# Kernel tuning notes

Measured on AMD Instinct MI355X. Metric: run time of the kernel, lower is better.

Reference implementation:

```python
import jax, jax.numpy as jnp
import numpy as np

N_NODES = 50000


def _sage_conv(x, src, dst, Wl, bl, Wr):
    # mean-aggregate source features onto targets (PyG SAGEConv, aggr='mean')
    msg = x[src]                                             # [E, C_in] gather
    s = jax.ops.segment_sum(msg, dst, num_segments=N_NODES)  # [N, C_in]
    cnt = jax.ops.segment_sum(jnp.ones((src.shape[0],), x.dtype), dst,
                              num_segments=N_NODES)          # [N]
    agg = s / jnp.maximum(cnt, 1.0)[:, None]
    # out = lin_l(agg) + lin_r(x); bias only on lin_l
    return agg @ Wl.T + bl + x @ Wr.T


def setup_inputs() -> dict:
    key = jax.random.key(0)
    ks = jax.random.split(key, 8)
    in_c, hid_c, out_c = 128, 128, 64
    n_edges = 800000
    x = jax.random.normal(ks[0], (N_NODES, in_c), dtype=jnp.float32)
    edge_index = jax.random.randint(ks[1], (2, n_edges), 0, N_NODES, dtype=jnp.int64)
    sc = lambda k, shp: jax.random.normal(k, shp, dtype=jnp.float32) / np.sqrt(shp[1])
    return {
        "x": x,
        "edge_index": edge_index,
        "W1l": sc(ks[2], (hid_c, in_c)),
        "b1l": jnp.zeros((hid_c,), jnp.float32),
        "W1r": sc(ks[3], (hid_c, in_c)),
        "W2l": sc(ks[4], (out_c, hid_c)),
        "b2l": jnp.zeros((out_c,), jnp.float32),
        "W2r": sc(ks[5], (out_c, hid_c)),
    }


def reference(x, edge_index, W1l, b1l, W1r, W2l, b2l, W2r):
    src, dst = edge_index[0], edge_index[1]
    h = jax.nn.relu(_sage_conv(x, src, dst, W1l, b1l, W1r))
    # dropout(p=0.5) is identity at inference (training=False)
    return _sage_conv(h, src, dst, W2l, b2l, W2r)
```

## Files before the change

### kernel.cpp

```cpp
#include <hip/hip_runtime.h>
#include <hip/hip_bf16.h>

#define N_NODES 50000
#define N_EDGES 800000
#define N_BUCKETS 196
#define BUCKET_CAP 8192
#define POISON 0xAAAAAAAAu

#define XCVT_BLK 6250
#define WCVT_BLK 48
#define EPB 2048
#define BKT_BLK 391

typedef __attribute__((ext_vector_type(8))) short short8;
typedef __attribute__((ext_vector_type(4))) float floatx4;

static __device__ __forceinline__ float bf16_lo(unsigned int v) {
  union { unsigned int u; float f; } c; c.u = v << 16; return c.f;
}
static __device__ __forceinline__ float bf16_hi(unsigned int v) {
  union { unsigned int u; float f; } c; c.u = v & 0xffff0000u; return c.f;
}
static __device__ __forceinline__ unsigned short f32_to_bf16_rne(float f) {
  union { float f; unsigned int u; } c; c.f = f;
  unsigned int u = c.u;
  unsigned int r = (u + 0x7fffu + ((u >> 16) & 1u)) >> 16;
  return (unsigned short)r;
}
static __device__ __forceinline__ unsigned int pack2(float a, float b) {
  return (unsigned int)f32_to_bf16_rne(a) | ((unsigned int)f32_to_bf16_rne(b) << 16);
}
static __device__ __forceinline__ uint2 pack4(float4 v) {
  return (uint2){pack2(v.x, v.y), pack2(v.z, v.w)};
}
static __device__ __forceinline__ void accum8(float* acc, uint4 v) {
  acc[0] += bf16_lo(v.x); acc[1] += bf16_hi(v.x);
  acc[2] += bf16_lo(v.y); acc[3] += bf16_hi(v.y);
  acc[4] += bf16_lo(v.z); acc[5] += bf16_hi(v.z);
  acc[6] += bf16_lo(v.w); acc[7] += bf16_hi(v.w);
}

__global__ __launch_bounds__(256) void prep_bucket_kernel(
    const float4* __restrict__ x4, uint2* __restrict__ xb4,
    const float4* __restrict__ w1l4, const float4* __restrict__ w1r4,
    const float4* __restrict__ w2l4, const float4* __restrict__ w2r4,
    uint2* __restrict__ o1l, uint2* __restrict__ o1r,
    uint2* __restrict__ o2l, uint2* __restrict__ o2r,
    const int* __restrict__ src, const int* __restrict__ dst,
    unsigned int* __restrict__ bcur, unsigned int* __restrict__ ebuf) {
  __shared__ int hist[N_BUCKETS];
  __shared__ int base[N_BUCKETS];
  const int b = blockIdx.x, tid = threadIdx.x;
  if (b < XCVT_BLK) {
    int i = b * 256 + tid;
    xb4[i] = pack4(x4[i]);
    return;
  }
  if (b < XCVT_BLK + WCVT_BLK) {
    int j = (b - XCVT_BLK) * 256 + tid;
    const float4* in; uint2* out; int o2, NJ;
    if (j < 4096)       { in = w1l4; out = o1l; o2 = j;         NJ = 128; }
    else if (j < 8192)  { in = w1r4; out = o1r; o2 = j - 4096;  NJ = 128; }
    else if (j < 10240) { in = w2l4; out = o2l; o2 = j - 8192;  NJ = 64; }
    else                { in = w2r4; out = o2r; o2 = j - 10240; NJ = 64; }
    int half = o2 & 1;
    int rest = o2 >> 1;
    int col  = rest % NJ;
    int qk   = rest / NJ;
    int quad = qk & 3, kb = qk >> 2;
    out[o2] = pack4(in[col * 32 + kb * 8 + quad * 2 + half]);
    return;
  }
  const int eb = b - XCVT_BLK - WCVT_BLK;
  for (int i = tid; i < N_BUCKETS; i += 256) hist[i] = 0;
  __syncthreads();
  const int e0 = eb * EPB;
  int bk[8], rk[8];
  unsigned int pk[8];
  bool val[8];
  #pragma unroll
  for (int k = 0; k < 8; ++k) {
    int e = e0 + k * 256 + tid;
    val[k] = (e < N_EDGES);
    if (val[k]) {
      int d = dst[e], s = src[e];
      bk[k] = d >> 8;
      pk[k] = ((unsigned int)(d & 255) << 16) | (unsigned int)s;
      rk[k] = atomicAdd(&hist[bk[k]], 1);
    }
  }
  __syncthreads();
  for (int i = tid; i < N_BUCKETS; i += 256) {
    int h = hist[i];
    base[i] = h ? (int)(atomicAdd(&bcur[i], (unsigned int)h) - POISON) : 0;
  }
  __syncthreads();
  #pragma unroll
  for (int k = 0; k < 8; ++k) {
    if (val[k]) {
      unsigned int p = (unsigned int)(base[bk[k]] + rk[k]);
      if (p < BUCKET_CAP) ebuf[(size_t)bk[k] * BUCKET_CAP + p] = pk[k];
    }
  }
}

__global__ __launch_bounds__(512) void local_csr_kernel(
    const unsigned int* __restrict__ ebuf, const unsigned int* __restrict__ bcur,
    int* __restrict__ start_g, int* __restrict__ cnt_g, int* __restrict__ eidx) {
  const int b = blockIdx.x;
  int nb = (int)(bcur[b] - POISON);
  nb = max(0, min(nb, BUCKET_CAP));
  __shared__ int cnt[256];
  __shared__ int loff[256];
  __shared__ int ws[4];
  if (threadIdx.x < 256) cnt[threadIdx.x] = 0;
  __syncthreads();
  const unsigned int* eb = ebuf + (size_t)b * BUCKET_CAP;
  for (int i = threadIdx.x; i < nb; i += 512)
    atomicAdd(&cnt[eb[i] >> 16], 1);
  __syncthreads();
  const int t256 = threadIdx.x & 255;
  const int lane = threadIdx.x & 63, wid = (threadIdx.x >> 6) & 3;
  int v = cnt[t256];
  int incl = v;
  #pragma unroll
  for (int d = 1; d < 64; d <<= 1) {
    int t = __shfl_up(incl, d, 64);
    if (lane >= d) incl += t;
  }
  if (threadIdx.x < 256 && lane == 63) ws[wid] = incl;
  __syncthreads();
  int add = 0;
  #pragma unroll
  for (int w = 0; w < 4; ++w) if (w < wid) add += ws[w];
  int excl = add + incl - v;
  if (threadIdx.x < 256) {
    loff[t256] = excl;
    int node = b * 256 + t256;
    if (node < N_NODES) {
      start_g[node] = b * BUCKET_CAP + excl;
      cnt_g[node] = v;
    }
  }
  __syncthreads();
  for (int i = threadIdx.x; i < nb; i += 512) {
    unsigned int p = eb[i];
    int pos = atomicAdd(&loff[p >> 16], 1);
    eidx[(size_t)b * BUCKET_CAP + pos] = (int)(p & 0xffffu);
  }
}

__global__ __launch_bounds__(256) void agg_gemm_kernel(
    const uint4* __restrict__ xb4,
    const int* __restrict__ start_g, const int* __restrict__ cnt_g,
    const int* __restrict__ eidx,
    const unsigned short* __restrict__ W1l, const unsigned short* __restrict__ W1r,
    const float* __restrict__ b1,
    const unsigned short* __restrict__ W2l, const unsigned short* __restrict__ W2r,
    const float* __restrict__ b2,
    unsigned short* __restrict__ z, unsigned short* __restrict__ rbuf) {
  __shared__ unsigned short lds_a[64 * 136];
  __shared__ unsigned short lds_x[64 * 136];
  const int tid = threadIdx.x, lane = tid & 63, wave = tid >> 6;
  const int quad = lane >> 4, r16 = lane & 15;
  const int cg = wave & 1, tw = wave >> 1;
  const int col0 = cg * 64;
  const int n0 = blockIdx.x * 64;

  #pragma unroll
  for (int k = 0; k < 4; ++k) {
    int idx = k * 256 + tid;
    int row = idx >> 4, col = idx & 15;
    int gr = n0 + row; if (gr >= N_NODES) gr = N_NODES - 1;
    ((uint4*)lds_x)[row * 17 + col] = xb4[(size_t)gr * 16 + col];
  }

  const int l16 = tid & 15;
  const int grp = tid >> 4;
  #pragma unroll 1
  for (int nn = 0; nn < 4; ++nn) {
    int row = nn * 16 + grp;
    int node = n0 + row;
    float acc[8];
    #pragma unroll
    for (int t = 0; t < 8; ++t) acc[t] = 0.f;
    int c = 0;
    if (node < N_NODES) {
      int e0 = start_g[node];
      c = cnt_g[node];
      int e1 = e0 + c;
      int e = e0;
      for (; e + 8 <= e1; e += 8) {
        int s[8];
        #pragma unroll
        for (int k = 0; k < 8; ++k) s[k] = eidx[e + k];
        uint4 v[8];
        #pragma unroll
        for (int k = 0; k < 8; ++k) v[k] = xb4[(size_t)s[k] * 16 + l16];
        #pragma unroll
        for (int k = 0; k < 8; ++k) accum8(acc, v[k]);
      }
      if (e + 4 <= e1) {
        int s[4];
        #pragma unroll
        for (int k = 0; k < 4; ++k) s[k] = eidx[e + k];
        uint4 v[4];
        #pragma unroll
        for (int k = 0; k < 4; ++k) v[k] = xb4[(size_t)s[k] * 16 + l16];
        #pragma unroll
        for (int k = 0; k < 4; ++k) accum8(acc, v[k]);
        e += 4;
      }
      for (; e < e1; ++e)
        accum8(acc, xb4[(size_t)eidx[e] * 16 + l16]);
    }
    float inv = 1.0f / fmaxf((float)c, 1.0f);
    uint4 o;
    o.x = pack2(acc[0] * inv, acc[1] * inv);
    o.y = pack2(acc[2] * inv, acc[3] * inv);
    o.z = pack2(acc[4] * inv, acc[5] * inv);
    o.w = pack2(acc[6] * inv, acc[7] * inv);
    *(uint4*)(lds_a + row * 136 + l16 * 8) = o;
  }
  __syncthreads();

  const unsigned short* As[2] = {lds_a, lds_x};
  const unsigned short* Ws[2] = {W1l, W1r};
  floatx4 acc1[2][4] = {};
  #pragma unroll
  for (int rt = 0; rt < 2; ++rt) {
    int lrow = tw * 32 + rt * 16;
    #pragma unroll
    for (int s = 0; s < 2; ++s) {
      const unsigned short* Ar = As[s] + (lrow + r16) * 136 + quad * 8;
      #pragma unroll
      for (int kb = 0; kb < 4; ++kb) {
        short8 a = *(const short8*)(Ar + kb * 32);
        const unsigned short* Wf = Ws[s] + ((size_t)(kb * 4 + quad) * 128) * 8;
        #pragma unroll
        for (int c = 0; c < 4; ++c) {
          short8 bfr = *(const short8*)(Wf + (size_t)(col0 + c * 16 + r16) * 8);
          acc1[rt][c] = __builtin_amdgcn_mfma_f32_16x16x32_bf16(a, bfr, acc1[rt][c], 0, 0, 0);
        }
      }
    }
  }
  __syncthreads();

  #pragma unroll
  for (int rt = 0; rt < 2; ++rt) {
    int lrow0 = tw * 32 + rt * 16 + quad * 4;
    #pragma unroll
    for (int c = 0; c < 4; ++c) {
      int j = col0 + c * 16 + r16;
      float bv = b1[j];
      #pragma unroll
      for (int r = 0; r < 4; ++r)
        lds_a[(lrow0 + r) * 136 + j] = f32_to_bf16_rne(fmaxf(acc1[rt][c][r] + bv, 0.f));
    }
  }
  __syncthreads();

  const unsigned short* W = cg ? W2r : W2l;
  unsigned short* outp = cg ? rbuf : z;
  #pragma unroll
  for (int rt = 0; rt < 2; ++rt) {
    int lrow = tw * 32 + rt * 16;
    floatx4 acc[4] = {};
    const unsigned short* la = lds_a + (lrow + r16) * 136 + quad * 8;
    #pragma unroll
    for (int kb = 0; kb < 4; ++kb) {
      short8 a = *(const short8*)(la + kb * 32);
      const unsigned short* Wf = W + ((size_t)(kb * 4 + quad) * 64) * 8;
      #pragma unroll
      for (int c = 0; c < 4; ++c) {
        short8 bfr = *(const short8*)(Wf + (size_t)(c * 16 + r16) * 8);
        acc[c] = __builtin_amdgcn_mfma_f32_16x16x32_bf16(a, bfr, acc[c], 0, 0, 0);
      }
    }
    int orow0 = n0 + lrow + quad * 4;
    #pragma unroll
    for (int c = 0; c < 4; ++c) {
      int j = c * 16 + r16;
      float bv = cg ? b2[j] : 0.f;
      #pragma unroll
      for (int r = 0; r < 4; ++r) {
        int node = orow0 + r;
        if (node < N_NODES)
          outp[(size_t)node * 64 + j] = f32_to_bf16_rne(acc[c][r] + bv);
      }
    }
  }
}

__global__ __launch_bounds__(256) void final_agg_kernel(
    const uint4* __restrict__ z4, const uint4* __restrict__ r4,
    const int* __restrict__ start_g, const int* __restrict__ cnt_g,
    const int* __restrict__ eidx, float* __restrict__ outp) {
  const int l8 = threadIdx.x & 7;
  const int node = blockIdx.x * 32 + (threadIdx.x >> 3);
  if (node >= N_NODES) return;
  int e0 = start_g[node];
  int c = cnt_g[node];
  int e1 = e0 + c;

  float acc[8];
  #pragma unroll
  for (int t = 0; t < 8; ++t) acc[t] = 0.f;

  int e = e0;
  for (; e + 8 <= e1; e += 8) {
    int s[8];
    #pragma unroll
    for (int k = 0; k < 8; ++k) s[k] = eidx[e + k];
    uint4 v[8];
    #pragma unroll
    for (int k = 0; k < 8; ++k) v[k] = z4[(size_t)s[k] * 8 + l8];
    #pragma unroll
    for (int k = 0; k < 8; ++k) accum8(acc, v[k]);
  }
  if (e + 4 <= e1) {
    int s[4];
    #pragma unroll
    for (int k = 0; k < 4; ++k) s[k] = eidx[e + k];
    uint4 v[4];
    #pragma unroll
    for (int k = 0; k < 4; ++k) v[k] = z4[(size_t)s[k] * 8 + l8];
    #pragma unroll
    for (int k = 0; k < 4; ++k) accum8(acc, v[k]);
    e += 4;
  }
  for (; e < e1; ++e)
    accum8(acc, z4[(size_t)eidx[e] * 8 + l8]);

  float inv = 1.0f / fmaxf((float)c, 1.0f);
  uint4 rv = r4[(size_t)node * 8 + l8];
  float4* op = (float4*)(outp + (size_t)node * 64 + l8 * 8);
  float4 a, b;
  a.x = acc[0] * inv + bf16_lo(rv.x); a.y = acc[1] * inv + bf16_hi(rv.x);
  a.z = acc[2] * inv + bf16_lo(rv.y); a.w = acc[3] * inv + bf16_hi(rv.y);
  b.x = acc[4] * inv + bf16_lo(rv.z); b.y = acc[5] * inv + bf16_hi(rv.z);
  b.z = acc[6] * inv + bf16_lo(rv.w); b.w = acc[7] * inv + bf16_hi(rv.w);
  op[0] = a; op[1] = b;
}

extern "C" void kernel_launch(void* const* d_in, const int* in_sizes, int n_in,
                              void* d_out, int out_size, void* d_ws, size_t ws_size,
                              hipStream_t stream) {
  (void)in_sizes; (void)n_in; (void)out_size; (void)ws_size;
  const float* x   = (const float*)d_in[0];
  const int*   ei  = (const int*)d_in[1];
  const float* W1l = (const float*)d_in[2];
  const float* b1l = (const float*)d_in[3];
  const float* W1r = (const float*)d_in[4];
  const float* W2l = (const float*)d_in[5];
  const float* b2l = (const float*)d_in[6];
  const float* W2r = (const float*)d_in[7];
  const int* src = ei;
  const int* dst = ei + N_EDGES;

  char* ws = (char*)d_ws;
  size_t p = 0;
  auto alloc = [&](size_t bytes) {
    char* q = ws + p;
    p = (p + bytes + 255) & ~(size_t)255;
    return q;
  };
  unsigned int* bcur = (unsigned int*)alloc((size_t)N_BUCKETS * 4);
  int* start_g = (int*)alloc((size_t)N_NODES * 4);
  int* cnt_g   = (int*)alloc((size_t)N_NODES * 4);
  unsigned int* ebuf = (unsigned int*)alloc((size_t)N_BUCKETS * BUCKET_CAP * 4);
  int* eidx    = (int*)alloc((size_t)N_BUCKETS * BUCKET_CAP * 4);
  unsigned short* xb   = (unsigned short*)alloc((size_t)N_NODES * 128 * 2);
  unsigned short* zb   = (unsigned short*)alloc((size_t)N_NODES * 64 * 2);
  unsigned short* rb   = (unsigned short*)alloc((size_t)N_NODES * 64 * 2);
  unsigned short* w1lb = (unsigned short*)alloc(128 * 128 * 2);
  unsigned short* w1rb = (unsigned short*)alloc(128 * 128 * 2);
  unsigned short* w2lb = (unsigned short*)alloc(64 * 128 * 2);
  unsigned short* w2rb = (unsigned short*)alloc(64 * 128 * 2);

  prep_bucket_kernel<<<XCVT_BLK + WCVT_BLK + BKT_BLK, 256, 0, stream>>>(
      (const float4*)x, (uint2*)xb,
      (const float4*)W1l, (const float4*)W1r, (const float4*)W2l, (const float4*)W2r,
      (uint2*)w1lb, (uint2*)w1rb, (uint2*)w2lb, (uint2*)w2rb,
      src, dst, bcur, (unsigned int*)ebuf);
  local_csr_kernel<<<N_BUCKETS, 512, 0, stream>>>(
      (const unsigned int*)ebuf, bcur, start_g, cnt_g, eidx);
  agg_gemm_kernel<<<(N_NODES + 63) / 64, 256, 0, stream>>>(
      (const uint4*)xb, start_g, cnt_g, eidx, w1lb, w1rb, b1l, w2lb, w2rb, b2l, zb, rb);
  final_agg_kernel<<<(N_NODES + 31) / 32, 256, 0, stream>>>(
      (const uint4*)zb, (const uint4*)rb, start_g, cnt_g, eidx, (float*)d_out);
}
```

Before: 189.6 us.

## Halve agg_gemm tile to 32 rows and stage edge indices in LDS

Cuts the agg_gemm block tile from 64 to 32 nodes, doubling the grid and shrinking per-block LDS so more blocks can be resident. Each block also copies its contiguous slice of CSR edge indices into shared memory up front and gathers from there. It falls back to global indices when the slice exceeds the LDS capacity. The aim is better latency hiding for the gather and fewer dependent global index loads, at the cost of an extra barrier, a prologue copy, and re-reading the weights in twice as many blocks.

```diff
diff --git a/kernel.cpp b/kernel.cpp
--- a/kernel.cpp
+++ b/kernel.cpp
@@ -11,6 +11,9 @@
 #define WCVT_BLK 48
 #define EPB 2048
 #define BKT_BLK 391
+
+#define TR 32
+#define ECAP 1536
 
 typedef __attribute__((ext_vector_type(8))) short short8;
 typedef __attribute__((ext_vector_type(4))) float floatx4;
@@ -159,26 +162,33 @@
     const unsigned short* __restrict__ W2l, const unsigned short* __restrict__ W2r,
     const float* __restrict__ b2,
     unsigned short* __restrict__ z, unsigned short* __restrict__ rbuf) {
-  __shared__ unsigned short lds_a[64 * 136];
-  __shared__ unsigned short lds_x[64 * 136];
+  __shared__ unsigned short lds_a[TR * 136];
+  __shared__ unsigned short lds_x[TR * 136];
+  __shared__ int eloc[ECAP];
   const int tid = threadIdx.x, lane = tid & 63, wave = tid >> 6;
   const int quad = lane >> 4, r16 = lane & 15;
   const int cg = wave & 1, tw = wave >> 1;
   const int col0 = cg * 64;
-  const int n0 = blockIdx.x * 64;
-
-  #pragma unroll
-  for (int k = 0; k < 4; ++k) {
+  const int n0 = blockIdx.x * TR;
+
+  #pragma unroll
+  for (int k = 0; k < (TR * 16) / 256; ++k) {
     int idx = k * 256 + tid;
     int row = idx >> 4, col = idx & 15;
     int gr = n0 + row; if (gr >= N_NODES) gr = N_NODES - 1;
     ((uint4*)lds_x)[row * 17 + col] = xb4[(size_t)gr * 16 + col];
   }
+  int nlast = n0 + TR - 1; if (nlast >= N_NODES) nlast = N_NODES - 1;
+  const int e_lo = start_g[n0];
+  const int e_hi = start_g[nlast] + cnt_g[nlast];
+  int ne = e_hi - e_lo; if (ne > ECAP) ne = ECAP; if (ne < 0) ne = 0;
+  for (int i = tid; i < ne; i += 256) eloc[i] = eidx[e_lo + i];
+  __syncthreads();
 
   const int l16 = tid & 15;
   const int grp = tid >> 4;
   #pragma unroll 1
-  for (int nn = 0; nn < 4; ++nn) {
+  for (int nn = 0; nn < TR / 16; ++nn) {
     int row = nn * 16 + grp;
     int node = n0 + row;
     float acc[8];
@@ -186,33 +196,49 @@
     for (int t = 0; t < 8; ++t) acc[t] = 0.f;
     int c = 0;
     if (node < N_NODES) {
-      int e0 = start_g[node];
+      int ge0 = start_g[node];
       c = cnt_g[node];
-      int e1 = e0 + c;
-      int e = e0;
-      for (; e + 8 <= e1; e += 8) {
-        int s[8];
-        #pragma unroll
-        for (int k = 0; k < 8; ++k) s[k] = eidx[e + k];
-        uint4 v[8];
-        #pragma unroll
-        for (int k = 0; k < 8; ++k) v[k] = xb4[(size_t)s[k] * 16 + l16];
-        #pragma unroll
-        for (int k = 0; k < 8; ++k) accum8(acc, v[k]);
+      int le0 = ge0 - e_lo;
+      if (le0 + c <= ne) {
+        int e = le0, e1 = le0 + c;
+        for (; e + 8 <= e1; e += 8) {
+          int s[8];
+          #pragma unroll
+          for (int k = 0; k < 8; ++k) s[k] = eloc[e + k];
+          uint4 v[8];
+          #pragma unroll
+          for (int k = 0; k < 8; ++k) v[k] = xb4[(size_t)s[k] * 16 + l16];
+          #pragma unroll
+          for (int k = 0; k < 8; ++k) accum8(acc, v[k]);
+        }
+        if (e + 4 <= e1) {
+          int s[4];
+          #pragma unroll
+          for (int k = 0; k < 4; ++k) s[k] = eloc[e + k];
+          uint4 v[4];
+          #pragma unroll
+          for (int k = 0; k < 4; ++k) v[k] = xb4[(size_t)s[k] * 16 + l16];
+          #pragma unroll
+          for (int k = 0; k < 4; ++k) accum8(acc, v[k]);
+          e += 4;
+        }
+        for (; e < e1; ++e)
+          accum8(acc, xb4[(size_t)eloc[e] * 16 + l16]);
+      } else {
+        int e = ge0, e1 = ge0 + c;
+        for (; e + 8 <= e1; e += 8) {
+          int s[8];
+          #pragma unroll
+          for (int k = 0; k < 8; ++k) s[k] = eidx[e + k];
+          uint4 v[8];
+          #pragma unroll
+          for (int k = 0; k < 8; ++k) v[k] = xb4[(size_t)s[k] * 16 + l16];
+          #pragma unroll
+          for (int k = 0; k < 8; ++k) accum8(acc, v[k]);
+        }
+        for (; e < e1; ++e)
+          accum8(acc, xb4[(size_t)eidx[e] * 16 + l16]);
       }
-      if (e + 4 <= e1) {
-        int s[4];
-        #pragma unroll
-        for (int k = 0; k < 4; ++k) s[k] = eidx[e + k];
-        uint4 v[4];
-        #pragma unroll
-        for (int k = 0; k < 4; ++k) v[k] = xb4[(size_t)s[k] * 16 + l16];
-        #pragma unroll
-        for (int k = 0; k < 4; ++k) accum8(acc, v[k]);
-        e += 4;
-      }
-      for (; e < e1; ++e)
-        accum8(acc, xb4[(size_t)eidx[e] * 16 + l16]);
     }
     float inv = 1.0f / fmaxf((float)c, 1.0f);
     uint4 o;
@@ -226,69 +252,61 @@
 
   const unsigned short* As[2] = {lds_a, lds_x};
   const unsigned short* Ws[2] = {W1l, W1r};
-  floatx4 acc1[2][4] = {};
-  #pragma unroll
-  for (int rt = 0; rt < 2; ++rt) {
-    int lrow = tw * 32 + rt * 16;
-    #pragma unroll
-    for (int s = 0; s < 2; ++s) {
-      const unsigned short* Ar = As[s] + (lrow + r16) * 136 + quad * 8;
+  floatx4 acc1[4] = {};
+  const int lrow = tw * 16;
+  #pragma unroll
+  for (int s = 0; s < 2; ++s) {
+    const unsigned short* Ar = As[s] + (lrow + r16) * 136 + quad * 8;
+    #pragma unroll
+    for (int kb = 0; kb < 4; ++kb) {
+      short8 a = *(const short8*)(Ar + kb * 32);
+      const unsigned short* Wf = Ws[s] + ((size_t)(kb * 4 + quad) * 128) * 8;
       #pragma unroll
-      for (int kb = 0; kb < 4; ++kb) {
-        short8 a = *(const short8*)(Ar + kb * 32);
-        const unsigned short* Wf = Ws[s] + ((size_t)(kb * 4 + quad) * 128) * 8;
-        #pragma unroll
-        for (int c = 0; c < 4; ++c) {
-          short8 bfr = *(const short8*)(Wf + (size_t)(col0 + c * 16 + r16) * 8);
-          acc1[rt][c] = __builtin_amdgcn_mfma_f32_16x16x32_bf16(a, bfr, acc1[rt][c], 0, 0, 0);
-        }
+      for (int c = 0; c < 4; ++c) {
+        short8 bfr = *(const short8*)(Wf + (size_t)(col0 + c * 16 + r16) * 8);
+        acc1[c] = __builtin_amdgcn_mfma_f32_16x16x32_bf16(a, bfr, acc1[c], 0, 0, 0);
       }
     }
   }
   __syncthreads();
 
-  #pragma unroll
-  for (int rt = 0; rt < 2; ++rt) {
-    int lrow0 = tw * 32 + rt * 16 + quad * 4;
+  {
+    int lrow0 = tw * 16 + quad * 4;
     #pragma unroll
     for (int c = 0; c < 4; ++c) {
       int j = col0 + c * 16 + r16;
       float bv = b1[j];
       #pragma unroll
       for (int r = 0; r < 4; ++r)
-        lds_a[(lrow0 + r) * 136 + j] = f32_to_bf16_rne(fmaxf(acc1[rt][c][r] + bv, 0.f));
+        lds_a[(lrow0 + r) * 136 + j] = f32_to_bf16_rne(fmaxf(acc1[c][r] + bv, 0.f));
     }
   }
   __syncthreads();
 
   const unsigned short* W = cg ? W2r : W2l;
   unsigned short* outp = cg ? rbuf : z;
-  #pragma unroll
-  for (int rt = 0; rt < 2; ++rt) {
-    int lrow = tw * 32 + rt * 16;
-    floatx4 acc[4] = {};
-    const unsigned short* la = lds_a + (lrow + r16) * 136 + quad * 8;
-    #pragma unroll
-    for (int kb = 0; kb < 4; ++kb) {
-      short8 a = *(const short8*)(la + kb * 32);
-      const unsigned short* Wf = W + ((size_t)(kb * 4 + quad) * 64) * 8;
-      #pragma unroll
-      for (int c = 0; c < 4; ++c) {
-        short8 bfr = *(const short8*)(Wf + (size_t)(c * 16 + r16) * 8);
-        acc[c] = __builtin_amdgcn_mfma_f32_16x16x32_bf16(a, bfr, acc[c], 0, 0, 0);
-      }
-    }
-    int orow0 = n0 + lrow + quad * 4;
+  floatx4 acc[4] = {};
+  const unsigned short* la = lds_a + (tw * 16 + r16) * 136 + quad * 8;
+  #pragma unroll
+  for (int kb = 0; kb < 4; ++kb) {
+    short8 a = *(const short8*)(la + kb * 32);
+    const unsigned short* Wf = W + ((size_t)(kb * 4 + quad) * 64) * 8;
     #pragma unroll
     for (int c = 0; c < 4; ++c) {
-      int j = c * 16 + r16;
-      float bv = cg ? b2[j] : 0.f;
-      #pragma unroll
-      for (int r = 0; r < 4; ++r) {
-        int node = orow0 + r;
-        if (node < N_NODES)
-          outp[(size_t)node * 64 + j] = f32_to_bf16_rne(acc[c][r] + bv);
-      }
+      short8 bfr = *(const short8*)(Wf + (size_t)(c * 16 + r16) * 8);
+      acc[c] = __builtin_amdgcn_mfma_f32_16x16x32_bf16(a, bfr, acc[c], 0, 0, 0);
+    }
+  }
+  int orow0 = n0 + tw * 16 + quad * 4;
+  #pragma unroll
+  for (int c = 0; c < 4; ++c) {
+    int j = c * 16 + r16;
+    float bv = cg ? b2[j] : 0.f;
+    #pragma unroll
+    for (int r = 0; r < 4; ++r) {
+      int node = orow0 + r;
+      if (node < N_NODES)
+        outp[(size_t)node * 64 + j] = f32_to_bf16_rne(acc[c][r] + bv);
     }
   }
 }
@@ -386,7 +404,7 @@
       src, dst, bcur, (unsigned int*)ebuf);
   local_csr_kernel<<<N_BUCKETS, 512, 0, stream>>>(
       (const unsigned int*)ebuf, bcur, start_g, cnt_g, eidx);
-  agg_gemm_kernel<<<(N_NODES + 63) / 64, 256, 0, stream>>>(
+  agg_gemm_kernel<<<(N_NODES + TR - 1) / TR, 256, 0, stream>>>(
       (const uint4*)xb, start_g, cnt_g, eidx, w1lb, w1rb, b1l, w2lb, w2rb, b2l, zb, rb);
   final_agg_kernel<<<(N_NODES + 31) / 32, 256, 0, stream>>>(
       (const uint4*)zb, (const uint4*)rb, start_g, cnt_g, eidx, (float*)d_out);
```

Measured after the change: 173.1 us. -8.7%, faster.
